# Kernel optimization log

Measured on AMD Instinct MI355X. Metric: run time of the kernel, lower is better.

The kernel has to match this reference:

```python
import jax, jax.numpy as jnp
import numpy as np

IN_CHN, OUT_CHN, KS = 256, 256, 3
STRIDE, PAD = 1, 1
T = 64                       # accumulator tile length
NBITS_ACC = 8                # b
NBITS_PSUM = NBITS_ACC - 3   # 5 -> Qn=-16, Qp=15
SHIFT = 4                    # shift_value for b=8 (default branch)


def _round_ste(x):
    # round with straight-through estimator (round_pass in torch code)
    return x + jax.lax.stop_gradient(jnp.round(x) - x)


def _oa(x, b):
    # bitwise overflow/wraparound correction (OA in torch code)
    mask = (1 << b) - 1
    half = 1 << (b - 1)
    qn, qp = -half, half - 1
    mid = (x >= qn) & (x <= qp)
    out = jnp.where(mid, x, 0.0)
    # torch .int() truncates toward zero; astype(int32) matches
    wrapped = (jnp.where(mid, 0.0, x).astype(jnp.int32) & mask).astype(x.dtype)
    # wrapped in [0, mask]; values > qp wrap down by 2*half (lower branch never fires)
    out3 = jnp.where(wrapped > qp, wrapped - 2.0 * half, wrapped)
    return out + out3


def setup_inputs() -> dict:
    key = jax.random.key(0)
    kx, kw = jax.random.split(key)
    x = jax.random.normal(kx, (4, IN_CHN, 56, 56), dtype=jnp.float32)
    weights = jax.random.uniform(kw, (OUT_CHN * IN_CHN * KS * KS, 1), dtype=jnp.float32) * 0.001
    return {"x": x, "weights": weights}


def reference(x, weights):
    W = weights.reshape(OUT_CHN, IN_CHN, KS, KS)
    # per-output-channel mean(|w|) scaling, detached
    scale = jax.lax.stop_gradient(jnp.mean(jnp.abs(W), axis=(1, 2, 3)))  # [Cout]
    wc = jnp.clip(W, -1.0, 1.0)
    bw = jax.lax.stop_gradient(jnp.sign(W) - wc) + wc  # sign with STE

    B, Cin, H, Wd = x.shape
    OH = (H - KS + 2 * PAD) // STRIDE + 1
    OW = (Wd - KS + 2 * PAD) // STRIDE + 1
    Kdim = Cin * KS * KS
    N = Kdim // T  # 2304 / 64 = 36 tiles, exact

    # im2col: (B, Cin*KS*KS, OH, OW), channel-major feature ordering == torch unfold
    patches = jax.lax.conv_general_dilated_patches(
        x, (KS, KS), (STRIDE, STRIDE), [(PAD, PAD), (PAD, PAD)])
    A = patches.reshape(B, Kdim, OH * OW).transpose(0, 2, 1)  # (B, L, K)
    X = bw.reshape(OUT_CHN, Kdim).T                            # (K, Cout)

    # tiled partial-sum matmul: psum[b,l,n,c] = sum_t A[b,l,n*T+t] * X[n*T+t,c]
    psum = jnp.einsum('blnt,ntc->blnc',
                      A.reshape(B, OH * OW, N, T),
                      X.reshape(N, T, OUT_CHN))

    qn = -2 ** (NBITS_PSUM - 1)
    qp = 2 ** (NBITS_PSUM - 1) - 1
    psum_q = _round_ste(jnp.clip(psum / (2.0 ** SHIFT), qn, qp))

    acc = psum_q.sum(axis=2).transpose(0, 2, 1)  # (B, Cout, L)
    out = _oa(acc, NBITS_ACC) * (2.0 ** SHIFT)
    out = out.reshape(B, OUT_CHN, OH, OW)
    return out * scale.reshape(1, -1, 1, 1)
```

## Files before the change

kernel.cpp:

```cpp
#include <hip/hip_runtime.h>

#define CIN      256
#define COUT     256
#define HWD      56
#define LSP      3136
#define BB       4
#define KDIM     2304
#define NT       36
#define BLTOT    12544
#define NBX      49
#define NTSB     (NT*NBX)

#define OFF_SCALE   0
#define OFF_HASEXC  1024
#define OFF_CNT     2048
#define OFF_EXC     38912
#define OFF_S       2398208
#define OFF_COMMON  4204544

__global__ __launch_bounds__(256)
void k_main(const float* __restrict__ x, const float* __restrict__ w,
            float* __restrict__ S, float* __restrict__ scale,
            int* __restrict__ has_exc, int* __restrict__ cnt,
            int* __restrict__ exc) {
    int id  = blockIdx.x;
    int tid = threadIdx.x;
    if (id < NTSB) {
        int n  = id / NBX;
        int bl = (id - n * NBX) * 256 + tid;
        int b  = bl / LSP;
        int l  = bl - b * LSP;
        int oh = l / HWD;
        int ow = l - oh * HWD;

        float m[9]; int off[9];
#pragma unroll
        for (int r = 0; r < 9; ++r) {
            int kh = r / 3, kw = r - 3 * (r / 3);
            int ih = oh - 1 + kh, iw = ow - 1 + kw;
            bool ok = ((unsigned)ih < (unsigned)HWD) & ((unsigned)iw < (unsigned)HWD);
            m[r]   = ok ? 1.f : 0.f;
            off[r] = ok ? (ih * HWD + iw) : 0;
        }

        int k0 = n * 64;
        int c0 = k0 / 9;
        int r0 = k0 - 9 * c0;
        const float* xc = x + (size_t)(b * CIN + c0) * LSP;

        float s = 0.f;
#pragma unroll
        for (int r = 0; r < 9; ++r)
            if (r >= r0) s = fmaf(m[r], xc[off[r]], s);
        xc += LSP;
#pragma unroll
        for (int cc = 0; cc < 6; ++cc) {
#pragma unroll
            for (int r = 0; r < 9; ++r) s = fmaf(m[r], xc[off[r]], s);
            xc += LSP;
        }
        if (r0 == 8) {
#pragma unroll
            for (int r = 0; r < 9; ++r) s = fmaf(m[r], xc[off[r]], s);
        } else {
#pragma unroll
            for (int r = 0; r < 9; ++r)
                if (r <= r0) s = fmaf(m[r], xc[off[r]], s);
        }
        S[n * BLTOT + bl] = s;
    } else {
        int c = id - NTSB;
        if (tid < NT) cnt[c * NT + tid] = 0;
        if (tid == 0) has_exc[c] = 0;
        __syncthreads();

        const float* wr = w + c * KDIM;
        float s = 0.f;
#pragma unroll
        for (int i = 0; i < 9; ++i) {
            int k = i * 256 + tid;
            float v = wr[k];
            s += fabsf(v);
            int sg = (v > 0.f) - (v < 0.f);
            if (sg != 1) {
                int n  = k >> 6;
                int ti = k & 63;
                int mag = 1 - sg;
                int idx = atomicAdd(&cnt[c * NT + n], 1);
                exc[(c * NT + n) * 64 + idx] = ti | (mag << 8);
                atomicOr(&has_exc[c], 1);
            }
        }
        __shared__ float red[256];
        red[tid] = s;
        __syncthreads();
#pragma unroll
        for (int o = 128; o > 0; o >>= 1) {
            if (tid < o) red[tid] += red[tid + o];
            __syncthreads();
        }
        if (tid == 0) scale[c] = red[0] * (1.f / (float)KDIM);
    }
}

__global__ __launch_bounds__(256)
void k_common(const float* __restrict__ S, float* __restrict__ common) {
    int bl = blockIdx.x * 256 + threadIdx.x;
    int acc = 0;
#pragma unroll
    for (int n = 0; n < NT; ++n) {
        float ps = S[n * BLTOT + bl] * 0.0625f;
        ps = fminf(fmaxf(ps, -16.f), 15.f);
        acc += (int)rintf(ps);
    }
    int w8 = ((acc + 128) & 255) - 128;
    common[bl] = (float)(w8 << 4);
}

__global__ __launch_bounds__(256)
void k_out(const float* __restrict__ x, const float* __restrict__ S,
           const float* __restrict__ common, const float* __restrict__ scale,
           const int* __restrict__ has_exc, const int* __restrict__ cnt,
           const int* __restrict__ exc, float* __restrict__ out) {
    int gid = blockIdx.x * 256 + threadIdx.x;
    int o4 = gid * 4;
    int l = o4 % LSP;
    int t = o4 / LSP;
    int c = t & 255;
    int b = t >> 8;

    float4 v;
    if (!has_exc[c]) {
        v = *(const float4*)&common[b * LSP + l];
    } else {
        float vv[4];
#pragma unroll
        for (int q = 0; q < 4; ++q) {
            int ll = l + q;
            int oh = ll / HWD, ow = ll - (ll / HWD) * HWD;
            int acc = 0;
            for (int n = 0; n < NT; ++n) {
                float ps = S[n * BLTOT + b * LSP + ll];
                int ct = cnt[c * NT + n];
                for (int e = 0; e < ct; ++e) {
                    int pk = exc[(c * NT + n) * 64 + e];
                    int ti = pk & 63;
                    int mag = pk >> 8;
                    int k = n * 64 + ti;
                    int ci = k / 9;
                    int r = k - 9 * ci;
                    int kh = r / 3;
                    int kw = r - 3 * kh;
                    int ih = oh - 1 + kh, iw = ow - 1 + kw;
                    float a = 0.f;
                    if ((unsigned)ih < (unsigned)HWD && (unsigned)iw < (unsigned)HWD)
                        a = x[(size_t)((b * CIN + ci) * HWD + ih) * HWD + iw];
                    ps -= (float)mag * a;
                }
                ps *= 0.0625f;
                ps = fminf(fmaxf(ps, -16.f), 15.f);
                acc += (int)rintf(ps);
            }
            int w8 = ((acc + 128) & 255) - 128;
            vv[q] = (float)(w8 << 4);
        }
        v = make_float4(vv[0], vv[1], vv[2], vv[3]);
    }
    float sc = scale[c];
    v.x *= sc; v.y *= sc; v.z *= sc; v.w *= sc;
    *(float4*)&out[o4] = v;
}

extern "C" void kernel_launch(void* const* d_in, const int* in_sizes, int n_in,
                              void* d_out, int out_size, void* d_ws, size_t ws_size,
                              hipStream_t stream) {
    const float* x = (const float*)d_in[0];
    const float* w = (const float*)d_in[1];
    float* out = (float*)d_out;

    char* ws = (char*)d_ws;
    float* scale   = (float*)(ws + OFF_SCALE);
    int*   has_exc = (int*)  (ws + OFF_HASEXC);
    int*   cnt     = (int*)  (ws + OFF_CNT);
    int*   exc     = (int*)  (ws + OFF_EXC);
    float* S       = (float*)(ws + OFF_S);
    float* common  = (float*)(ws + OFF_COMMON);

    k_main<<<NTSB + COUT, 256, 0, stream>>>(x, w, S, scale, has_exc, cnt, exc);
    k_common<<<BLTOT / 256, 256, 0, stream>>>(S, common);
    k_out<<<(BB * COUT * LSP) / (4 * 256), 256, 0, stream>>>(
        x, S, common, scale, has_exc, cnt, exc, out);
}
```

Baseline: 86.05 us.

## Fuse common-value reduction into output kernel, one block per 32 positions

Merges k_common and k_out into a single kernel. Each block computes the quantized per-position accumulator for 32 spatial positions in shared memory, then writes all 256 output channels for those positions. This drops one launch and the global round-trip through the common buffer. In exchange, output writes become strided across channels (32-float runs per channel), and there are only 392 blocks, which may reduce store coalescing and occupancy.

```diff
diff --git a/kernel.cpp b/kernel.cpp
--- a/kernel.cpp
+++ b/kernel.cpp
@@ -10,13 +10,13 @@
 #define BLTOT    12544
 #define NBX      49
 #define NTSB     (NT*NBX)
+#define PPB      32
 
 #define OFF_SCALE   0
 #define OFF_HASEXC  1024
 #define OFF_CNT     2048
 #define OFF_EXC     38912
 #define OFF_S       2398208
-#define OFF_COMMON  4204544
 
 __global__ __launch_bounds__(256)
 void k_main(const float* __restrict__ x, const float* __restrict__ w,
@@ -104,71 +104,89 @@
 }
 
 __global__ __launch_bounds__(256)
-void k_common(const float* __restrict__ S, float* __restrict__ common) {
-    int bl = blockIdx.x * 256 + threadIdx.x;
-    int acc = 0;
-#pragma unroll
-    for (int n = 0; n < NT; ++n) {
-        float ps = S[n * BLTOT + bl] * 0.0625f;
-        ps = fminf(fmaxf(ps, -16.f), 15.f);
-        acc += (int)rintf(ps);
-    }
-    int w8 = ((acc + 128) & 255) - 128;
-    common[bl] = (float)(w8 << 4);
-}
-
-__global__ __launch_bounds__(256)
-void k_out(const float* __restrict__ x, const float* __restrict__ S,
-           const float* __restrict__ common, const float* __restrict__ scale,
-           const int* __restrict__ has_exc, const int* __restrict__ cnt,
-           const int* __restrict__ exc, float* __restrict__ out) {
-    int gid = blockIdx.x * 256 + threadIdx.x;
-    int o4 = gid * 4;
-    int l = o4 % LSP;
-    int t = o4 / LSP;
-    int c = t & 255;
-    int b = t >> 8;
-
-    float4 v;
-    if (!has_exc[c]) {
-        v = *(const float4*)&common[b * LSP + l];
-    } else {
-        float vv[4];
-#pragma unroll
-        for (int q = 0; q < 4; ++q) {
-            int ll = l + q;
-            int oh = ll / HWD, ow = ll - (ll / HWD) * HWD;
-            int acc = 0;
-            for (int n = 0; n < NT; ++n) {
-                float ps = S[n * BLTOT + b * LSP + ll];
-                int ct = cnt[c * NT + n];
-                for (int e = 0; e < ct; ++e) {
-                    int pk = exc[(c * NT + n) * 64 + e];
-                    int ti = pk & 63;
-                    int mag = pk >> 8;
-                    int k = n * 64 + ti;
-                    int ci = k / 9;
-                    int r = k - 9 * ci;
-                    int kh = r / 3;
-                    int kw = r - 3 * kh;
-                    int ih = oh - 1 + kh, iw = ow - 1 + kw;
-                    float a = 0.f;
-                    if ((unsigned)ih < (unsigned)HWD && (unsigned)iw < (unsigned)HWD)
-                        a = x[(size_t)((b * CIN + ci) * HWD + ih) * HWD + iw];
-                    ps -= (float)mag * a;
+void k_out2(const float* __restrict__ x, const float* __restrict__ S,
+            const float* __restrict__ scale, const int* __restrict__ has_exc,
+            const int* __restrict__ cnt, const int* __restrict__ exc,
+            float* __restrict__ out) {
+    __shared__ int   q[NT][PPB];
+    __shared__ float cv[PPB];
+    __shared__ float sscale[COUT];
+    __shared__ int   she[COUT];
+
+    int t   = threadIdx.x;
+    int bl0 = blockIdx.x * PPB;
+    int b   = bl0 / LSP;
+    int l0  = bl0 - b * LSP;
+
+    sscale[t] = scale[t];
+    she[t]    = has_exc[t];
+
+    int p  = t & 31;
+    int nb = t >> 5;
+#pragma unroll
+    for (int i = 0; i < 5; ++i) {
+        int nn = nb + 8 * i;
+        if (nn < NT) {
+            float ps = S[nn * BLTOT + bl0 + p] * 0.0625f;
+            ps = fminf(fmaxf(ps, -16.f), 15.f);
+            q[nn][p] = (int)rintf(ps);
+        }
+    }
+    __syncthreads();
+    if (t < PPB) {
+        int acc = 0;
+#pragma unroll
+        for (int n = 0; n < NT; ++n) acc += q[n][t];
+        int w8 = ((acc + 128) & 255) - 128;
+        cv[t] = (float)(w8 << 4);
+    }
+    __syncthreads();
+
+#pragma unroll
+    for (int cc = 0; cc < 8; ++cc) {
+        int c  = (t >> 3) + 32 * cc;
+        int p4 = (t & 7) * 4;
+        float sc = sscale[c];
+        float4 v;
+        if (!she[c]) {
+            v = make_float4(cv[p4], cv[p4 + 1], cv[p4 + 2], cv[p4 + 3]);
+        } else {
+            float vv[4];
+#pragma unroll
+            for (int j = 0; j < 4; ++j) {
+                int ll = l0 + p4 + j;
+                int oh = ll / HWD, ow = ll - (ll / HWD) * HWD;
+                int acc = 0;
+                for (int n = 0; n < NT; ++n) {
+                    float ps = S[n * BLTOT + b * LSP + ll];
+                    int ct = cnt[c * NT + n];
+                    for (int e = 0; e < ct; ++e) {
+                        int pk = exc[(c * NT + n) * 64 + e];
+                        int ti = pk & 63;
+                        int mag = pk >> 8;
+                        int k = n * 64 + ti;
+                        int ci = k / 9;
+                        int r  = k - 9 * ci;
+                        int kh = r / 3;
+                        int kw = r - 3 * kh;
+                        int ih = oh - 1 + kh, iw = ow - 1 + kw;
+                        float a = 0.f;
+                        if ((unsigned)ih < (unsigned)HWD && (unsigned)iw < (unsigned)HWD)
+                            a = x[(size_t)((b * CIN + ci) * HWD + ih) * HWD + iw];
+                        ps -= (float)mag * a;
+                    }
+                    ps *= 0.0625f;
+                    ps = fminf(fmaxf(ps, -16.f), 15.f);
+                    acc += (int)rintf(ps);
                 }
-                ps *= 0.0625f;
-                ps = fminf(fmaxf(ps, -16.f), 15.f);
-                acc += (int)rintf(ps);
+                int w8 = ((acc + 128) & 255) - 128;
+                vv[j] = (float)(w8 << 4);
             }
-            int w8 = ((acc + 128) & 255) - 128;
-            vv[q] = (float)(w8 << 4);
-        }
-        v = make_float4(vv[0], vv[1], vv[2], vv[3]);
-    }
-    float sc = scale[c];
-    v.x *= sc; v.y *= sc; v.z *= sc; v.w *= sc;
-    *(float4*)&out[o4] = v;
+            v = make_float4(vv[0], vv[1], vv[2], vv[3]);
+        }
+        v.x *= sc; v.y *= sc; v.z *= sc; v.w *= sc;
+        *(float4*)&out[(size_t)(b * COUT + c) * LSP + l0 + p4] = v;
+    }
 }
 
 extern "C" void kernel_launch(void* const* d_in, const int* in_sizes, int n_in,
@@ -184,10 +202,7 @@
     int*   cnt     = (int*)  (ws + OFF_CNT);
     int*   exc     = (int*)  (ws + OFF_EXC);
     float* S       = (float*)(ws + OFF_S);
-    float* common  = (float*)(ws + OFF_COMMON);
 
     k_main<<<NTSB + COUT, 256, 0, stream>>>(x, w, S, scale, has_exc, cnt, exc);
-    k_common<<<BLTOT / 256, 256, 0, stream>>>(S, common);
-    k_out<<<(BB * COUT * LSP) / (4 * 256), 256, 0, stream>>>(
-        x, S, common, scale, has_exc, cnt, exc, out);
+    k_out2<<<BLTOT / PPB, 256, 0, stream>>>(x, S, scale, has_exc, cnt, exc, out);
 }
```

After: 85.43 us. No clear change (-0.7%).
